# Optimization experiments

Hardware: AMD Instinct MI355X
Metric: run time of the kernel (lower is better)

The kernel has to match this reference:

```python
import jax, jax.numpy as jnp
import numpy as np

EPS = 1e-5
NUM_HEADS = 8
KEY_DIM = 32
V_DIM = 128  # att_ratio * key_dim

def bn2d(x, g, b, m, v):
    # inference BatchNorm2d on NCHW
    s = g * jax.lax.rsqrt(v + EPS)
    return x * s[None, :, None, None] + (b - m * s)[None, :, None, None]

def conv1x1(x, w):
    # w: [out_c, in_c], x: [B,C,H,W]
    return jnp.einsum('oc,bchw->bohw', w, x)

def _bn_params(key, c):
    k1, k2, k3, k4 = jax.random.split(key, 4)
    g = jax.random.uniform(k1, (c,), jnp.float32, 0.5, 1.5)
    b = jax.random.normal(k2, (c,), jnp.float32) * 0.1
    m = jax.random.normal(k3, (c,), jnp.float32) * 0.1
    v = jax.random.uniform(k4, (c,), jnp.float32, 0.5, 1.5)
    return g, b, m, v

def setup_inputs() -> dict:
    key = jax.random.key(0)
    ks = jax.random.split(key, 12)
    inp_dim, out_dim = 256, 512
    kv_out = (KEY_DIM + V_DIM) * NUM_HEADS      # 1280
    q_out = KEY_DIM * NUM_HEADS                 # 256
    merge_dim = V_DIM * NUM_HEADS               # 1024
    hid = out_dim * 2                            # mlp_ratio=2 -> 1024
    d = {}
    d['x'] = jax.random.normal(ks[0], (32, inp_dim, 32, 32), jnp.float32)
    d['kv_w'] = jax.random.normal(ks[1], (kv_out, inp_dim), jnp.float32) * 0.02
    d['kv_g'], d['kv_b'], d['kv_m'], d['kv_v'] = _bn_params(ks[2], kv_out)
    d['q_w'] = jax.random.normal(ks[3], (q_out, inp_dim), jnp.float32) * 0.02
    d['q_g'], d['q_b'], d['q_m'], d['q_v'] = _bn_params(ks[4], q_out)
    d['mg_w'] = jax.random.normal(ks[5], (out_dim, merge_dim), jnp.float32) * 0.02
    d['mg_g'], d['mg_b'], d['mg_m'], d['mg_v'] = _bn_params(ks[6], out_dim)
    d['fc1_w'] = jax.random.normal(ks[7], (hid, out_dim), jnp.float32) * 0.02
    d['bn1_g'], d['bn1_b'], d['bn1_m'], d['bn1_v'] = _bn_params(ks[8], hid)
    d['fc2_w'] = jax.random.normal(ks[9], (out_dim, hid), jnp.float32) * 0.02
    d['bn2_g'], d['bn2_b'], d['bn2_m'], d['bn2_v'] = _bn_params(ks[10], out_dim)
    return d

def reference(x, kv_w, kv_g, kv_b, kv_m, kv_v, q_w, q_g, q_b, q_m, q_v,
              mg_w, mg_g, mg_b, mg_m, mg_v,
              fc1_w, bn1_g, bn1_b, bn1_m, bn1_v,
              fc2_w, bn2_g, bn2_b, bn2_m, bn2_v):
    B, C, H, W = x.shape
    scale = KEY_DIM ** (-0.5)
    # kv projection: conv1x1 + BN, then split per head into k, v
    kv = bn2d(conv1x1(x, kv_w), kv_g, kv_b, kv_m, kv_v)
    kv = kv.reshape(B, NUM_HEADS, KEY_DIM + V_DIM, H * W)
    k = kv[:, :, :KEY_DIM]   # [B,h,Dk,N]
    v = kv[:, :, KEY_DIM:]   # [B,h,Dv,N]
    # query subsampling: AvgPool2d(kernel=1, stride=2) == strided slice
    xq = x[:, :, ::2, ::2]
    q = bn2d(conv1x1(xq, q_w), q_g, q_b, q_m, q_v)
    q = q.reshape(B, NUM_HEADS, KEY_DIM, -1)  # [B,h,Dk,Nq]
    # att = q^T @ k * scale, softmax over keys
    att = jax.nn.softmax(jnp.einsum('bhdq,bhdn->bhqn', q, k) * scale, axis=-1)
    h2, w2 = (H + 1) // 2, (W + 1) // 2
    # out = v @ att^T, channel-first layout
    o = jnp.einsum('bhvn,bhqn->bhvq', v, att).reshape(B, NUM_HEADS * V_DIM, h2, w2)
    # merge: GELU -> conv1x1 -> BN
    o = bn2d(conv1x1(jax.nn.gelu(o, approximate=False), mg_w), mg_g, mg_b, mg_m, mg_v)
    # ConvMlp: conv1x1 -> BN -> GELU -> conv1x1 -> BN
    y = bn2d(conv1x1(o, fc1_w), bn1_g, bn1_b, bn1_m, bn1_v)
    y = jax.nn.gelu(y, approximate=False)
    y = bn2d(conv1x1(y, fc2_w), bn2_g, bn2_b, bn2_m, bn2_v)
    return y
```

## Files before the change

### kernel.cpp

```cpp
#include <hip/hip_runtime.h>
#include <hip/hip_bf16.h>

#define BN_EPS 1e-5f

typedef short s8v __attribute__((ext_vector_type(8)));
typedef float f4v __attribute__((ext_vector_type(4)));
typedef unsigned short u16x8 __attribute__((ext_vector_type(8)));

__device__ __forceinline__ float bu2f(unsigned short u) {
    union { unsigned int i; float f; } c; c.i = ((unsigned int)u) << 16; return c.f;
}
__device__ __forceinline__ unsigned short f2bu(float f) {
    union { float f; unsigned int i; } c; c.f = f;
    unsigned int i = c.i;
    i += 0x7FFFu + ((i >> 16) & 1u);
    return (unsigned short)(i >> 16);
}
__device__ __forceinline__ float gelu_exact(float x) {
    return 0.5f * x * (1.0f + erff(x * 0.70710678118654752f));
}
__device__ __forceinline__ float ldin(const void* p, long i, bool f32) {
    return f32 ? ((const float*)p)[i] : bu2f(((const unsigned short*)p)[i]);
}
__device__ __forceinline__ s8v ldfrag(const unsigned short* p) {
    return *reinterpret_cast<const s8v*>(p);
}
__device__ __forceinline__ void gld16(const void* g, void* l) {
    __builtin_amdgcn_global_load_lds(
        (const __attribute__((address_space(1))) unsigned int*)g,
        (__attribute__((address_space(3))) unsigned int*)l, 16, 0, 0);
}
__device__ __forceinline__ s8v ldsw32(const unsigned short* T, int row, int quad) {
    return *reinterpret_cast<const s8v*>(T + row * 32 + ((quad ^ ((row >> 1) & 3)) << 3));
}
__device__ __forceinline__ s8v ldsw64(const unsigned short* T, int row, int chunk) {
    return *reinterpret_cast<const s8v*>(T + row * 64 + ((chunk ^ (row & 7)) << 3));
}
__device__ __forceinline__ int detect_f32(const unsigned short* xu) {
    int insane = 0;
    for (int i = 0; i < 128; ++i) {
        unsigned int e = (xu[i] >> 7) & 0xFFu;
        if (e == 255u || (e != 0u && (e < 96u || e > 159u))) ++insane;
    }
    return (insane >= 16) ? 1 : 0;
}

__global__ __launch_bounds__(256)
void prep_kernel(const void* __restrict__ x,
                 const void* __restrict__ w0, const void* __restrict__ w1,
                 const void* __restrict__ w2, const void* __restrict__ w3,
                 const void* __restrict__ w4,
                 unsigned short* __restrict__ wdst,
                 unsigned short* __restrict__ xT,
                 unsigned short* __restrict__ xqT,
                 int* __restrict__ dtf)
{
    __shared__ int sflag;
    __shared__ unsigned short T[64][66];
    const int tid = threadIdx.x;
    const int bid = blockIdx.x;
    if (tid == 0) {
        int fl = detect_f32((const unsigned short*)x);
        sflag = fl;
        if (bid == 0) *dtf = fl;
    }
    __syncthreads();
    const bool f = (sflag != 0);

    if (bid < 960) {
        long idx = (long)bid * 2048 + tid * 8;
        const void* s; long off;
        if      (idx <  327680L) { s = w0; off = idx; }
        else if (idx <  393216L) { s = w1; off = idx - 327680L; }
        else if (idx <  917504L) { s = w2; off = idx - 393216L; }
        else if (idx < 1441792L) { s = w3; off = idx - 917504L; }
        else                     { s = w4; off = idx - 1441792L; }
        u16x8 pk;
        if (f) {
            float4 a = *((const float4*)((const float*)s + off));
            float4 b = *((const float4*)((const float*)s + off + 4));
            pk[0]=f2bu(a.x); pk[1]=f2bu(a.y); pk[2]=f2bu(a.z); pk[3]=f2bu(a.w);
            pk[4]=f2bu(b.x); pk[5]=f2bu(b.y); pk[6]=f2bu(b.z); pk[7]=f2bu(b.w);
        } else {
            pk = *((const u16x8*)((const unsigned short*)s + off));
        }
        *reinterpret_cast<u16x8*>(wdst + idx) = pk;
        return;
    }
    int b, c0, n0, ND; bool SUBS;
    if (bid < 3008) { int t = bid - 960;  b = t >> 6; int r = t & 63;
                      c0 = (r >> 4) * 64; n0 = (r & 15) * 64; ND = 1024; SUBS = false; }
    else            { int t = bid - 3008; b = t >> 4; int r = t & 15;
                      c0 = (r >> 2) * 64; n0 = (r & 3) * 64;  ND = 256;  SUBS = true; }
    unsigned short* dst = SUBS ? xqT : xT;
    {
        int nn = tid & 63, cq = tid >> 6;
        int n = n0 + nn;
        int sc = SUBS ? ((n >> 4) * 64 + (n & 15) * 2) : n;
        long base = ((long)b * 256 + c0 + cq * 16) * 1024 + sc;
        #pragma unroll
        for (int i = 0; i < 16; ++i)
            T[nn][cq * 16 + i] = f2bu(ldin(x, base + (long)i * 1024, f));
    }
    __syncthreads();
    {
        int cc = tid & 63, nq = tid >> 6;
        #pragma unroll
        for (int i = 0; i < 16; ++i) {
            int nn = nq * 16 + i;
            dst[((long)b * ND + n0 + nn) * 256 + c0 + cc] = T[nn][cc];
        }
    }
}

template<int OUT_MODE, bool DO_GELU, bool PRESCALE, int BM>
__global__ __launch_bounds__(256)
void mfma_gemm(const unsigned short* __restrict__ A,
               const unsigned short* __restrict__ B,
               const void* __restrict__ gg, const void* __restrict__ bb,
               const void* __restrict__ mmu, const void* __restrict__ vv,
               void* __restrict__ out0, unsigned short* __restrict__ out1,
               int M, int K, int N, const int* __restrict__ dtflag)
{
    constexpr int NF = (BM == 128) ? 4 : 2;
    __shared__ unsigned short As[BM * 64];
    __shared__ unsigned short Bs[128 * 64];
    __shared__ float sS[BM], sO[BM];

    const bool wf = (*dtflag != 0);
    const int tid = threadIdx.x;
    const int lane = tid & 63;
    const int wave = tid >> 6;
    const int quad = lane >> 4;
    const int l15  = lane & 15;
    const int wm2 = (BM == 128) ? (wave >> 1) * 64 : 0;
    const int wn2 = (BM == 128) ? (wave & 1) * 64 : wave * 32;
    const int b  = blockIdx.z;
    const int bm = blockIdx.y * BM;
    const int bn = blockIdx.x * 128;

    if (tid < BM) {
        int m = bm + tid;
        float g  = ldin(gg,  m, wf), be = ldin(bb,  m, wf);
        float mu = ldin(mmu, m, wf), va = ldin(vv,  m, wf);
        float s = g * rsqrtf(va + BN_EPS);
        float o = be - mu * s;
        if (PRESCALE) { s *= 0.17677669529663687f; o *= 0.17677669529663687f; }
        sS[tid] = s; sO[tid] = o;
    }

    const unsigned short* Bb = B + (long)b * N * K;

    f4v acc[4][NF];
    #pragma unroll
    for (int i = 0; i < 4; ++i)
        #pragma unroll
        for (int j = 0; j < NF; ++j) acc[i][j] = (f4v){0.f, 0.f, 0.f, 0.f};

    const int lr8 = lane >> 3;
    const int lc8 = lane & 7;

    for (int k0 = 0; k0 < K; k0 += 64) {
        #pragma unroll
        for (int j = 0; j < (BM == 128 ? 4 : 2); ++j) {
            int base = wave * (BM == 128 ? 32 : 16) + j * 8;
            int r = base + lr8;
            gld16(A + (long)(bm + r) * K + k0 + ((lc8 ^ (r & 7)) << 3),
                  As + base * 64);
        }
        #pragma unroll
        for (int j = 0; j < 4; ++j) {
            int base = wave * 32 + j * 8;
            int r = base + lr8;
            gld16(Bb + (long)(bn + r) * K + k0 + ((lc8 ^ (r & 7)) << 3),
                  Bs + base * 64);
        }
        __syncthreads();

        #pragma unroll
        for (int sk = 0; sk < 2; ++sk) {
            s8v af[4], bfr[NF];
            #pragma unroll
            for (int i = 0; i < 4; ++i)
                af[i]  = ldsw64(As, wm2 + i * 16 + l15, sk * 4 + quad);
            #pragma unroll
            for (int j = 0; j < NF; ++j)
                bfr[j] = ldsw64(Bs, wn2 + j * 16 + l15, sk * 4 + quad);
            #pragma unroll
            for (int i = 0; i < 4; ++i)
                #pragma unroll
                for (int j = 0; j < NF; ++j)
                    acc[i][j] = __builtin_amdgcn_mfma_f32_16x16x32_bf16(
                        af[i], bfr[j], acc[i][j], 0, 0, 0);
        }
        __syncthreads();
    }

    #pragma unroll
    for (int i = 0; i < 4; ++i) {
        int m0l = wm2 + i * 16 + quad * 4;
        int m0  = bm + m0l;
        float s0 = sS[m0l + 0], o0 = sO[m0l + 0];
        float s1 = sS[m0l + 1], o1 = sO[m0l + 1];
        float s2 = sS[m0l + 2], o2 = sO[m0l + 2];
        float s3 = sS[m0l + 3], o3 = sO[m0l + 3];
        #pragma unroll
        for (int j = 0; j < NF; ++j) {
            int n = bn + wn2 + j * 16 + l15;
            float v0 = acc[i][j][0] * s0 + o0;
            float v1 = acc[i][j][1] * s1 + o1;
            float v2 = acc[i][j][2] * s2 + o2;
            float v3 = acc[i][j][3] * s3 + o3;
            if (DO_GELU) {
                v0 = gelu_exact(v0); v1 = gelu_exact(v1);
                v2 = gelu_exact(v2); v3 = gelu_exact(v3);
            }
            if (OUT_MODE == 0) {
                ushort4 pk; pk.x = f2bu(v0); pk.y = f2bu(v1);
                pk.z = f2bu(v2); pk.w = f2bu(v3);
                *reinterpret_cast<ushort4*>(
                    (unsigned short*)out0 + ((long)b * N + n) * M + m0) = pk;
            } else if (OUT_MODE == 1) {
                int h = m0 / 160, seg = m0 - h * 160;
                if (seg < 32) {
                    ushort4 pk; pk.x = f2bu(v0); pk.y = f2bu(v1);
                    pk.z = f2bu(v2); pk.w = f2bu(v3);
                    *reinterpret_cast<ushort4*>(
                        (unsigned short*)out0 + ((long)(b * 8 + h) * 1024 + n) * 32 + seg) = pk;
                } else {
                    long vb = (((long)b * 8 + h) * 128 + (seg - 32)) * N + n;
                    out1[vb + 0 * N] = f2bu(v0);
                    out1[vb + 1 * N] = f2bu(v1);
                    out1[vb + 2 * N] = f2bu(v2);
                    out1[vb + 3 * N] = f2bu(v3);
                }
            } else if (OUT_MODE == 2) {
                int b2 = n >> 8, nl = n & 255;
                long ob = ((long)b2 * M + m0) * 256 + nl;
                if (wf) {
                    ((float*)out0)[ob + 0L * 256] = v0;
                    ((float*)out0)[ob + 1L * 256] = v1;
                    ((float*)out0)[ob + 2L * 256] = v2;
                    ((float*)out0)[ob + 3L * 256] = v3;
                } else {
                    ((unsigned short*)out0)[ob + 0L * 256] = f2bu(v0);
                    ((unsigned short*)out0)[ob + 1L * 256] = f2bu(v1);
                    ((unsigned short*)out0)[ob + 2L * 256] = f2bu(v2);
                    ((unsigned short*)out0)[ob + 3L * 256] = f2bu(v3);
                }
            } else {
                int h = m0 >> 5;
                ushort4 pk; pk.x = f2bu(v0); pk.y = f2bu(v1);
                pk.z = f2bu(v2); pk.w = f2bu(v3);
                *reinterpret_cast<ushort4*>(
                    (unsigned short*)out0 + ((long)(b * 8 + h) * 256 + n) * 32 + (m0 & 31)) = pk;
            }
        }
    }
}

__global__ __launch_bounds__(512, 4)
void attn_mfma(const unsigned short* __restrict__ kvK,
               const unsigned short* __restrict__ kvV,
               const unsigned short* __restrict__ qh,
               unsigned short* __restrict__ goT)
{
    __shared__ unsigned short Ks[64 * 32];
    __shared__ unsigned short Vs[128 * 64];
    __shared__ unsigned short Ps[128][72];
    __shared__ float redS[128];

    const int tid = threadIdx.x;
    const int lane = tid & 63;
    const int wave = tid >> 6;
    const int quad = lane >> 4;
    const int l15  = lane & 15;
    const int h    = blockIdx.x;
    const int b    = blockIdx.y;
    const int q0   = blockIdx.z * 128;
    const int wq   = wave * 16;

    const unsigned short* Qb = qh  + (long)(b * 8 + h) * 256 * 32;
    const unsigned short* Kb = kvK + (long)(b * 8 + h) * 1024 * 32;
    const unsigned short* Vb = kvV + (long)(b * 8 + h) * 128 * 1024;

    s8v qf = ldfrag(Qb + (long)(q0 + wq + l15) * 32 + quad * 8);

    f4v o[8];
    #pragma unroll
    for (int i = 0; i < 8; ++i) o[i] = (f4v){0.f, 0.f, 0.f, 0.f};
    float rs[4] = {0.f, 0.f, 0.f, 0.f};

    for (int n0 = 0; n0 < 1024; n0 += 64) {
        if (wave < 4) {
            int r = wave * 16 + (lane >> 2);
            int c = (lane & 3) ^ ((r >> 1) & 3);
            gld16(Kb + (long)(n0 + r) * 32 + (c << 3), Ks + wave * 16 * 32);
        }
        {
            int rb = wave * 16;
            int r0 = rb + (lane >> 3), r1 = r0 + 8;
            int s  = lane & 7;
            gld16(Vb + (long)r0 * 1024 + n0 + ((s ^ (r0 & 7)) << 3), Vs + rb * 64);
            gld16(Vb + (long)r1 * 1024 + n0 + ((s ^ (r1 & 7)) << 3), Vs + (rb + 8) * 64);
        }
        __syncthreads();

        #pragma unroll
        for (int j = 0; j < 4; ++j) {
            s8v kf = ldsw32(Ks, j * 16 + l15, quad);
            f4v z = (f4v){0.f, 0.f, 0.f, 0.f};
            f4v sa = __builtin_amdgcn_mfma_f32_16x16x32_bf16(qf, kf, z, 0, 0, 0);
            #pragma unroll
            for (int r = 0; r < 4; ++r) {
                float p = __expf(fminf(sa[r], 30.f));
                rs[r] += p;
                Ps[wq + quad * 4 + r][j * 16 + l15] = f2bu(p);
            }
        }
        #pragma unroll
        for (int ks = 0; ks < 2; ++ks) {
            s8v pf = ldfrag(&Ps[wq + l15][ks * 32 + quad * 8]);
            #pragma unroll
            for (int i = 0; i < 8; ++i) {
                s8v vf = ldsw64(Vs, i * 16 + l15, ks * 4 + quad);
                o[i] = __builtin_amdgcn_mfma_f32_16x16x32_bf16(vf, pf, o[i], 0, 0, 0);
            }
        }
        __syncthreads();
    }

    #pragma unroll
    for (int r = 0; r < 4; ++r) {
        float s = rs[r];
        s += __shfl_xor(s, 1);
        s += __shfl_xor(s, 2);
        s += __shfl_xor(s, 4);
        s += __shfl_xor(s, 8);
        if (l15 == 0) redS[wq + quad * 4 + r] = s;
    }
    float linv = 1.0f / redS[wq + l15];
    int q = q0 + wq + l15;
    #pragma unroll
    for (int i = 0; i < 8; ++i) {
        ushort4 pk;
        pk.x = f2bu(gelu_exact(o[i][0] * linv));
        pk.y = f2bu(gelu_exact(o[i][1] * linv));
        pk.z = f2bu(gelu_exact(o[i][2] * linv));
        pk.w = f2bu(gelu_exact(o[i][3] * linv));
        *reinterpret_cast<ushort4*>(
            goT + ((long)b * 256 + q) * 1024 + h * 128 + i * 16 + quad * 4) = pk;
    }
}

extern "C" void kernel_launch(void* const* d_in, const int* in_sizes, int n_in,
                              void* d_out, int out_size, void* d_ws, size_t ws_size,
                              hipStream_t stream)
{
    const void* x     = d_in[0];
    const void* kv_w  = d_in[1];
    const void* kv_g  = d_in[2];  const void* kv_b  = d_in[3];
    const void* kv_m  = d_in[4];  const void* kv_v  = d_in[5];
    const void* q_w   = d_in[6];
    const void* q_g   = d_in[7];  const void* q_b   = d_in[8];
    const void* q_m   = d_in[9];  const void* q_v   = d_in[10];
    const void* mg_w  = d_in[11];
    const void* mg_g  = d_in[12]; const void* mg_b  = d_in[13];
    const void* mg_m  = d_in[14]; const void* mg_v  = d_in[15];
    const void* fc1_w = d_in[16];
    const void* bn1_g = d_in[17]; const void* bn1_b = d_in[18];
    const void* bn1_m = d_in[19]; const void* bn1_v = d_in[20];
    const void* fc2_w = d_in[21];
    const void* bn2_g = d_in[22]; const void* bn2_b = d_in[23];
    const void* bn2_m = d_in[24]; const void* bn2_v = d_in[25];

    unsigned short* ws  = (unsigned short*)d_ws;
    int*            dtf = (int*)d_ws;
    unsigned short* wsW  = ws + 8;
    unsigned short* wKV  = wsW;
    unsigned short* wQ   = wsW + 327680L;
    unsigned short* wMG  = wsW + 393216L;
    unsigned short* wFC1 = wsW + 917504L;
    unsigned short* wFC2 = wsW + 1441792L;
    unsigned short* xT   = ws + 1966088L;
    unsigned short* goT  = xT;
    unsigned short* xqT  = ws + 10354696L;
    unsigned short* qhb  = ws + 12451848L;
    unsigned short* kvK  = ws + 14549000L;
    unsigned short* kvV  = ws + 22937608L;
    unsigned short* y1T  = kvV;
    unsigned short* y2T  = kvV + 4194304L;

    dim3 blk(256, 1, 1);

    prep_kernel<<<3520, blk, 0, stream>>>(
        x, kv_w, q_w, mg_w, fc1_w, fc2_w, wsW, xT, xqT, dtf);

    mfma_gemm<3, false, true, 64><<<dim3(2, 4, 32), blk, 0, stream>>>(
        wQ, xqT, q_g, q_b, q_m, q_v, qhb, nullptr, 256, 256, 256, dtf);

    mfma_gemm<1, false, false, 128><<<dim3(8, 10, 32), blk, 0, stream>>>(
        wKV, xT, kv_g, kv_b, kv_m, kv_v, kvK, kvV, 1280, 256, 1024, dtf);

    attn_mfma<<<dim3(8, 32, 2), dim3(512, 1, 1), 0, stream>>>(kvK, kvV, qhb, goT);

    mfma_gemm<0, false, false, 64><<<dim3(64, 8, 1), blk, 0, stream>>>(
        wMG, goT, mg_g, mg_b, mg_m, mg_v, y1T, nullptr, 512, 1024, 8192, dtf);

    mfma_gemm<0, true, false, 64><<<dim3(64, 16, 1), blk, 0, stream>>>(
        wFC1, y1T, bn1_g, bn1_b, bn1_m, bn1_v, y2T, nullptr, 1024, 512, 8192, dtf);

    mfma_gemm<2, false, false, 64><<<dim3(64, 8, 1), blk, 0, stream>>>(
        wFC2, y2T, bn2_g, bn2_b, bn2_m, bn2_v, d_out, nullptr, 512, 1024, 8192, dtf);
}
```

Measured before the change: 306.4 us.

## Double-buffer GEMM LDS tiles with K=32 steps and paired-row swizzle

Reworks the MFMA GEMM main loop to keep two LDS buffers, issuing async global-to-LDS loads for the next K slice while the current slice is being multiplied. The K step shrinks from 64 to 32 so the two buffers fit in the same LDS footprint. A new paired-row swizzle packs two 32-wide rows into each 64-element LDS line to limit bank conflicts. The cost is one barrier per 32-wide K step instead of two per 64-wide step, with fewer MFMAs between barriers.

```diff
diff --git a/kernel.cpp b/kernel.cpp
--- a/kernel.cpp
+++ b/kernel.cpp
@@ -35,6 +35,19 @@
 }
 __device__ __forceinline__ s8v ldsw64(const unsigned short* T, int row, int chunk) {
     return *reinterpret_cast<const s8v*>(T + row * 64 + ((chunk ^ (row & 7)) << 3));
+}
+__device__ __forceinline__ s8v ldpr(const unsigned short* T, int row, int q) {
+    int g = row >> 1;
+    return *reinterpret_cast<const s8v*>(
+        T + g * 64 + ((((row & 1) << 2) | (q ^ (g & 3))) << 3));
+}
+__device__ __forceinline__ void stage_pair(const unsigned short* src, int rowBase,
+                                           int K, int k0, unsigned short* dstBase,
+                                           int gbase, int lane) {
+    int g = gbase + (lane >> 3);
+    int R = 2 * g + ((lane & 7) >> 2);
+    int c = (lane & 3) ^ (g & 3);
+    gld16(src + (long)(rowBase + R) * K + k0 + (c << 3), dstBase + gbase * 64);
 }
 __device__ __forceinline__ int detect_f32(const unsigned short* xu) {
     int insane = 0;
@@ -123,8 +136,10 @@
                int M, int K, int N, const int* __restrict__ dtflag)
 {
     constexpr int NF = (BM == 128) ? 4 : 2;
-    __shared__ unsigned short As[BM * 64];
-    __shared__ unsigned short Bs[128 * 64];
+    constexpr int AG = BM / 2;
+    constexpr int ACALLS = (BM == 128) ? 2 : 1;
+    __shared__ __align__(16) unsigned short As[2][AG * 64];
+    __shared__ __align__(16) unsigned short Bs[2][64 * 64];
     __shared__ float sS[BM], sO[BM];
 
     const bool wf = (*dtflag != 0);
@@ -157,42 +172,39 @@
         #pragma unroll
         for (int j = 0; j < NF; ++j) acc[i][j] = (f4v){0.f, 0.f, 0.f, 0.f};
 
-    const int lr8 = lane >> 3;
-    const int lc8 = lane & 7;
-
-    for (int k0 = 0; k0 < K; k0 += 64) {
-        #pragma unroll
-        for (int j = 0; j < (BM == 128 ? 4 : 2); ++j) {
-            int base = wave * (BM == 128 ? 32 : 16) + j * 8;
-            int r = base + lr8;
-            gld16(A + (long)(bm + r) * K + k0 + ((lc8 ^ (r & 7)) << 3),
-                  As + base * 64);
-        }
-        #pragma unroll
-        for (int j = 0; j < 4; ++j) {
-            int base = wave * 32 + j * 8;
-            int r = base + lr8;
-            gld16(Bb + (long)(bn + r) * K + k0 + ((lc8 ^ (r & 7)) << 3),
-                  Bs + base * 64);
-        }
-        __syncthreads();
-
-        #pragma unroll
-        for (int sk = 0; sk < 2; ++sk) {
-            s8v af[4], bfr[NF];
+    #pragma unroll
+    for (int j = 0; j < ACALLS; ++j)
+        stage_pair(A, bm, K, 0, As[0], wave * (AG / 4) + j * 8, lane);
+    #pragma unroll
+    for (int j = 0; j < 2; ++j)
+        stage_pair(Bb, bn, K, 0, Bs[0], wave * 16 + j * 8, lane);
+    __syncthreads();
+
+    const int NT = K >> 5;
+    for (int t = 0; t < NT; ++t) {
+        const int cur = t & 1;
+        if (t + 1 < NT) {
+            const int k1 = (t + 1) << 5;
             #pragma unroll
-            for (int i = 0; i < 4; ++i)
-                af[i]  = ldsw64(As, wm2 + i * 16 + l15, sk * 4 + quad);
+            for (int j = 0; j < ACALLS; ++j)
+                stage_pair(A, bm, K, k1, As[cur ^ 1], wave * (AG / 4) + j * 8, lane);
+            #pragma unroll
+            for (int j = 0; j < 2; ++j)
+                stage_pair(Bb, bn, K, k1, Bs[cur ^ 1], wave * 16 + j * 8, lane);
+        }
+        s8v af[4], bfr[NF];
+        #pragma unroll
+        for (int i = 0; i < 4; ++i)
+            af[i]  = ldpr(As[cur], wm2 + i * 16 + l15, quad);
+        #pragma unroll
+        for (int j = 0; j < NF; ++j)
+            bfr[j] = ldpr(Bs[cur], wn2 + j * 16 + l15, quad);
+        #pragma unroll
+        for (int i = 0; i < 4; ++i)
             #pragma unroll
             for (int j = 0; j < NF; ++j)
-                bfr[j] = ldsw64(Bs, wn2 + j * 16 + l15, sk * 4 + quad);
-            #pragma unroll
-            for (int i = 0; i < 4; ++i)
-                #pragma unroll
-                for (int j = 0; j < NF; ++j)
-                    acc[i][j] = __builtin_amdgcn_mfma_f32_16x16x32_bf16(
-                        af[i], bfr[j], acc[i][j], 0, 0, 0);
-        }
+                acc[i][j] = __builtin_amdgcn_mfma_f32_16x16x32_bf16(
+                    af[i], bfr[j], acc[i][j], 0, 0, 0);
         __syncthreads();
     }
 
```

New measurement: 329.5 us. 7.5% more time.
